# Optimization experiments

Measured on AMD Instinct MI355X. Metric: run time of the kernel, lower is better.

Reference implementation:

```python
import jax, jax.numpy as jnp
import numpy as np

B, N_MM, N_V, N_A = 2, 256, 64, 128
DIM, HEADS, ATTN_RATIO, MLP_RATIO = 1024, 16, 0.25, 4.0
INNER = int(DIM * ATTN_RATIO)          # 256
HID = int(DIM * MLP_RATIO)             # 4096
SCALE = (DIM // HEADS) ** -0.5         # faithful to source: uses dim//num_heads
EPS = 1e-5


def setup_inputs() -> dict:
    key = jax.random.key(0)
    ks = jax.random.split(key, 16)
    s = 0.02
    return {
        "xmm": jax.random.normal(ks[0], (B, N_MM, DIM), jnp.float32),
        "xv": jax.random.normal(ks[1], (B, N_V, DIM), jnp.float32),
        "xa": jax.random.normal(ks[2], (B, N_A, DIM), jnp.float32),
        "ln_mm_w": jnp.ones((DIM,), jnp.float32),
        "ln_mm_b": jnp.zeros((DIM,), jnp.float32),
        "ln_v_w": jnp.ones((DIM,), jnp.float32),
        "ln_v_b": jnp.zeros((DIM,), jnp.float32),
        "ln_a_w": jnp.ones((DIM,), jnp.float32),
        "ln_a_b": jnp.zeros((DIM,), jnp.float32),
        "Wq": jax.random.normal(ks[3], (DIM, INNER), jnp.float32) * s,
        "Wkv": jax.random.normal(ks[4], (2 * DIM, 2 * INNER), jnp.float32) * s,
        "Wproj": jax.random.normal(ks[5], (INNER, DIM), jnp.float32) * s,
        "bproj": jnp.zeros((DIM,), jnp.float32),
        "ln_mlp_w": jnp.ones((DIM,), jnp.float32),
        "ln_mlp_b": jnp.zeros((DIM,), jnp.float32),
        "W1": jax.random.normal(ks[6], (DIM, HID), jnp.float32) * s,
        "b1": jnp.zeros((HID,), jnp.float32),
        "W2": jax.random.normal(ks[7], (HID, DIM), jnp.float32) * s,
        "b2": jnp.zeros((DIM,), jnp.float32),
    }


def _ln(x, w, b):
    m = x.mean(-1, keepdims=True)
    v = ((x - m) ** 2).mean(-1, keepdims=True)
    return (x - m) / jnp.sqrt(v + EPS) * w + b


def reference(xmm, xv, xa, ln_mm_w, ln_mm_b, ln_v_w, ln_v_b, ln_a_w, ln_a_b,
              Wq, Wkv, Wproj, bproj, ln_mlp_w, ln_mlp_b, W1, b1, W2, b2):
    hd = INNER // HEADS
    src_mm = _ln(xmm, ln_mm_w, ln_mm_b)
    src_v = _ln(xv, ln_v_w, ln_v_b)
    src_a = _ln(xa, ln_a_w, ln_a_b)

    # kv(x_va) where x_va = cat([xv broadcast over N_a, xa broadcast over N_v], -1).
    # Equivalent to projecting each stream separately and broadcast-adding:
    kv_v = src_v @ Wkv[:DIM]            # [B, N_v, 2*INNER]
    kv_a = src_a @ Wkv[DIM:]            # [B, N_a, 2*INNER]
    kv = kv_v[:, :, None, :] + kv_a[:, None, :, :]          # [B, N_v, N_a, 2*INNER]
    kv = kv.reshape(B, N_V * N_A, 2, HEADS, hd)
    k = kv[:, :, 0].transpose(0, 2, 1, 3)                   # [B, H, N_va, hd]
    v = kv[:, :, 1].transpose(0, 2, 1, 3)

    q = (src_mm @ Wq).reshape(B, N_MM, HEADS, hd).transpose(0, 2, 1, 3)

    attn = jnp.einsum('bhqd,bhkd->bhqk', q, k) * SCALE
    attn = jax.nn.softmax(attn, axis=-1)
    out = jnp.einsum('bhqk,bhkd->bhqd', attn, v)
    out = out.transpose(0, 2, 1, 3).reshape(B, N_MM, INNER)
    out = out @ Wproj + bproj

    xmm = xmm + out
    h = _ln(xmm, ln_mlp_w, ln_mlp_b)
    h = jax.nn.gelu(h @ W1 + b1, approximate=False) @ W2 + b2
    return xmm + h
```

## Files before the change

kernel.cpp:

```cpp
#include <hip/hip_runtime.h>
#include <hip/hip_bf16.h>
#include <math.h>


typedef unsigned short ushort_t;
typedef __attribute__((ext_vector_type(8))) __bf16 bf16x8;
typedef __attribute__((ext_vector_type(4))) float f32x4;

#define DEVFN static __device__ __forceinline__

DEVFN ushort_t f2bf(float f) {
    unsigned int x = __float_as_uint(f);
    unsigned int r = x + 0x7FFFu + ((x >> 16) & 1u);
    return (ushort_t)(r >> 16);
}
DEVFN void unpack8(uint4 dv, float* dst) {
    unsigned int ws[4] = {dv.x, dv.y, dv.z, dv.w};
#pragma unroll
    for (int i = 0; i < 4; i++) {
        dst[2 * i] = __uint_as_float(ws[i] << 16);
        dst[2 * i + 1] = __uint_as_float(ws[i] & 0xFFFF0000u);
    }
}

DEVFN void ln_body(const float* __restrict__ x, const float* __restrict__ w,
                   const float* __restrict__ b, ushort_t* __restrict__ out,
                   int row) {
    const float4* xr4 = (const float4*)(x + (size_t)row * 1024);
    ushort_t* orow = out + (size_t)row * 1024;
    int tid = threadIdx.x;
    float4 v4 = xr4[tid];
    float s = v4.x + v4.y + v4.z + v4.w;
    float ss = v4.x * v4.x + v4.y * v4.y + v4.z * v4.z + v4.w * v4.w;
#pragma unroll
    for (int off = 32; off > 0; off >>= 1) {
        s += __shfl_down(s, off);
        ss += __shfl_down(ss, off);
    }
    __shared__ float red[8];
    if ((tid & 63) == 0) {
        red[tid >> 6] = s;
        red[4 + (tid >> 6)] = ss;
    }
    __syncthreads();
    s = red[0] + red[1] + red[2] + red[3];
    ss = red[4] + red[5] + red[6] + red[7];
    float mean = s * (1.f / 1024.f);
    float var = ss * (1.f / 1024.f) - mean * mean;
    float rstd = rsqrtf(var + 1e-5f);
    const float4 w4 = ((const float4*)w)[tid];
    const float4 b4 = ((const float4*)b)[tid];
    union { ushort_t u[4]; uint2 v; } pk;
    pk.u[0] = f2bf((v4.x - mean) * rstd * w4.x + b4.x);
    pk.u[1] = f2bf((v4.y - mean) * rstd * w4.y + b4.y);
    pk.u[2] = f2bf((v4.z - mean) * rstd * w4.z + b4.z);
    pk.u[3] = f2bf((v4.w - mean) * rstd * w4.w + b4.w);
    *(uint2*)(&orow[tid * 4]) = pk.v;
}

struct LNSeg {
    const float* x; const float* w; const float* b; ushort_t* out; int start;
};
struct TDesc { const float* in; ushort_t* out; int R, C, nx, start; };

DEVFN void transpose_body(TDesc d, int t, ushort_t* lds) {
    int bx = (t % d.nx) * 64;
    int by = (t / d.nx) * 64;
    int tid = threadIdx.x;
#pragma unroll
    for (int it = 0; it < 4; it++) {
        int idx = it * 256 + tid;
        int r = idx >> 4;
        int c4 = (idx & 15) << 2;
        float4 v = *(const float4*)(&d.in[(size_t)(by + r) * d.C + bx + c4]);
        float vals[4] = {v.x, v.y, v.z, v.w};
#pragma unroll
        for (int j = 0; j < 4; j++) {
            int c = c4 + j;
            int rs = (r + (((c >> 2) & 7) << 3)) & 63;
            lds[c * 64 + rs] = f2bf(vals[j]);
        }
    }
    __syncthreads();
#pragma unroll
    for (int it = 0; it < 2; it++) {
        int idx = it * 256 + tid;
        int c = idx >> 3;
        int l8 = idx & 7;
        int rs = ((l8 << 3) + (((c >> 2) & 7) << 3)) & 63;
        uint4 val = *(const uint4*)(&lds[c * 64 + rs]);
        *(uint4*)(&d.out[(size_t)(bx + c) * d.R + by + (l8 << 3)]) = val;
    }
    __syncthreads();
}

__global__ __launch_bounds__(256) void prep_kernel(LNSeg l0, LNSeg l1,
                                                   LNSeg l2, TDesc d0,
                                                   TDesc d1) {
    int id = blockIdx.x;
    if (id < 896) {
        LNSeg s = (id >= l2.start) ? l2 : ((id >= l1.start) ? l1 : l0);
        ln_body(s.x, s.w, s.b, s.out, id - s.start);
        return;
    }
    id -= 896;
    __shared__ ushort_t tile[64 * 64];
    TDesc d = (id >= d1.start) ? d1 : d0;
    transpose_body(d, id - d.start, tile);
}

template <int EPI, typename OutT>
DEVFN void gemm64_core(const ushort_t* __restrict__ A, int lda,
                       const ushort_t* __restrict__ B, int ldb,
                       OutT* __restrict__ C, int ldc,
                       const float* __restrict__ bias,
                       const float* __restrict__ resid, int K, int m0, int n0,
                       ushort_t* As, ushort_t* Bs,
                       float* __restrict__ stats = nullptr) {
    constexpr int LS = 72;
    int tid = threadIdx.x;
    int wave = tid >> 6, lane = tid & 63;
    int wm = wave >> 1, wn = wave & 1;
    int quad = lane >> 4, l16 = lane & 15;

    f32x4 acc[2][2];
#pragma unroll
    for (int i = 0; i < 2; i++)
#pragma unroll
        for (int j = 0; j < 2; j++) acc[i][j] = (f32x4){0.f, 0.f, 0.f, 0.f};

    int r = tid >> 3;
    int c = tid & 7;
    const ushort_t* Ap = A + (size_t)(m0 + r) * lda + c * 8;
    const ushort_t* Bp = B + (size_t)(n0 + r) * ldb + c * 8;
    const ushort_t* Ap2 = Ap + (size_t)32 * lda;
    const ushort_t* Bp2 = Bp + (size_t)32 * ldb;
    uint4 ra = *(const uint4*)Ap, ra2 = *(const uint4*)Ap2;
    uint4 rb = *(const uint4*)Bp, rb2 = *(const uint4*)Bp2;

    for (int k0 = 0; k0 < K; k0 += 64) {
        *(uint4*)(&As[r * LS + c * 8]) = ra;
        *(uint4*)(&As[(r + 32) * LS + c * 8]) = ra2;
        *(uint4*)(&Bs[r * LS + c * 8]) = rb;
        *(uint4*)(&Bs[(r + 32) * LS + c * 8]) = rb2;
        __syncthreads();
        if (k0 + 64 < K) {
            ra = *(const uint4*)(Ap + k0 + 64);
            ra2 = *(const uint4*)(Ap2 + k0 + 64);
            rb = *(const uint4*)(Bp + k0 + 64);
            rb2 = *(const uint4*)(Bp2 + k0 + 64);
        }
#pragma unroll
        for (int ks = 0; ks < 2; ks++) {
            bf16x8 af[2], bfr[2];
#pragma unroll
            for (int i = 0; i < 2; i++)
                af[i] = *(const bf16x8*)(
                    &As[(wm * 32 + i * 16 + l16) * LS + ks * 32 + quad * 8]);
#pragma unroll
            for (int j = 0; j < 2; j++)
                bfr[j] = *(const bf16x8*)(
                    &Bs[(wn * 32 + j * 16 + l16) * LS + ks * 32 + quad * 8]);
#pragma unroll
            for (int i = 0; i < 2; i++)
#pragma unroll
                for (int j = 0; j < 2; j++)
                    acc[i][j] = __builtin_amdgcn_mfma_f32_16x16x32_bf16(
                        af[i], bfr[j], acc[i][j], 0, 0, 0);
        }
        __syncthreads();
    }

    float srow[2][4] = {{0.f, 0.f, 0.f, 0.f}, {0.f, 0.f, 0.f, 0.f}};
    float ssrow[2][4] = {{0.f, 0.f, 0.f, 0.f}, {0.f, 0.f, 0.f, 0.f}};

#pragma unroll
    for (int i = 0; i < 2; i++)
#pragma unroll
        for (int j = 0; j < 2; j++) {
            int col = n0 + wn * 32 + j * 16 + l16;
            int rbase = m0 + wm * 32 + i * 16 + quad * 4;
            float bv = (EPI == 5) ? bias[col] : 0.f;
#pragma unroll
            for (int rr = 0; rr < 4; rr++) {
                int row = rbase + rr;
                float vv = acc[i][j][rr] + bv;
                if constexpr (EPI == 5) {
                    vv += resid[(size_t)row * ldc + col];
                    srow[i][rr] += vv;
                    ssrow[i][rr] += vv * vv;
                }
                if constexpr (sizeof(OutT) == 2)
                    C[(size_t)row * ldc + col] = (OutT)f2bf(vv);
                else
                    C[(size_t)row * ldc + col] = vv;
            }
        }

    if constexpr (EPI == 5) {
        float* ls = (float*)As;
#pragma unroll
        for (int i = 0; i < 2; i++)
#pragma unroll
            for (int rr = 0; rr < 4; rr++) {
                float s = srow[i][rr], ss = ssrow[i][rr];
#pragma unroll
                for (int m = 1; m < 16; m <<= 1) {
                    s += __shfl_xor(s, m);
                    ss += __shfl_xor(ss, m);
                }
                if (l16 == 0) {
                    int rl = wm * 32 + i * 16 + quad * 4 + rr;
                    ls[rl * 4 + wn * 2 + 0] = s;
                    ls[rl * 4 + wn * 2 + 1] = ss;
                }
            }
        __syncthreads();
        if (tid < 64) {
            float s = ls[tid * 4 + 0] + ls[tid * 4 + 2];
            float ss = ls[tid * 4 + 1] + ls[tid * 4 + 3];
            stats[(size_t)(m0 + tid) * 2 + 0] = s;
            stats[(size_t)(m0 + tid) * 2 + 1] = ss;
        }
    }
}

struct GSeg {
    const ushort_t* A; const ushort_t* B; ushort_t* C;
    int lda, ldb, ldc, nx, start;
};

__global__ __launch_bounds__(256) void projT_kernel(GSeg s0, GSeg s1, GSeg s2,
                                                    TDesc d0, TDesc d1,
                                                    TDesc d2, int K) {
    __shared__ ushort_t As[64 * 72];
    __shared__ ushort_t Bs[64 * 72];
    int id = blockIdx.x;
    if (id < 80) {
        GSeg s = (id >= s2.start) ? s2 : ((id >= s1.start) ? s1 : s0);
        int t = id - s.start;
        int n0 = (t % s.nx) * 64;
        int m0 = (t / s.nx) * 64;
        gemm64_core<0, ushort_t>(s.A, s.lda, s.B, s.ldb, s.C, s.ldc, nullptr,
                                 nullptr, K, m0, n0, As, Bs);
        return;
    }
    id -= 80;
    TDesc d = (id >= d2.start) ? d2 : ((id >= d1.start) ? d1 : d0);
    transpose_body(d, id - d.start, As);
}

__global__ __launch_bounds__(256) void ygemm_kernel(
    const ushort_t* __restrict__ A, const ushort_t* __restrict__ Bt,
    float* __restrict__ y, const float* __restrict__ bproj,
    const float* __restrict__ xmm, float* __restrict__ pstats) {
    __shared__ ushort_t As[64 * 72];
    __shared__ ushort_t Bs[64 * 72];
    gemm64_core<5, float>(A, 256, Bt, 256, y, 1024, bproj, xmm, 256,
                          blockIdx.y * 64, blockIdx.x * 64, As, Bs,
                          pstats + (size_t)blockIdx.x * 512 * 2);
}

__global__ __launch_bounds__(256) void mlp1_kernel(
    const float* __restrict__ y, const float* __restrict__ pstats,
    const float* __restrict__ lnw, const float* __restrict__ lnb,
    const ushort_t* __restrict__ W1t, const float* __restrict__ b1,
    ushort_t* __restrict__ g) {
    constexpr int LS = 40;
    __shared__ ushort_t As[64 * LS];
    __shared__ ushort_t Bs[64 * LS];
    __shared__ float wls[1024], bls[1024];
    int tid = threadIdx.x;
    int m0 = blockIdx.y * 64, n0 = blockIdx.x * 64;

    ((float4*)wls)[tid] = ((const float4*)lnw)[tid];
    ((float4*)bls)[tid] = ((const float4*)lnb)[tid];

    int r = tid >> 2, c = tid & 3;
    float s = 0.f, ss = 0.f;
#pragma unroll
    for (int k = 0; k < 4; k++) {
        size_t o = ((size_t)(c * 4 + k) * 512 + (m0 + r)) * 2;
        s += pstats[o];
        ss += pstats[o + 1];
    }
    s += __shfl_xor(s, 1); ss += __shfl_xor(ss, 1);
    s += __shfl_xor(s, 2); ss += __shfl_xor(ss, 2);
    float mr = s * (1.f / 1024.f);
    float var = ss * (1.f / 1024.f) - mr * mr;
    float rs = rsqrtf(var + 1e-5f);

    int wave = tid >> 6, lane = tid & 63;
    int wm = wave >> 1, wn = wave & 1;
    int quad = lane >> 4, l16 = lane & 15;

    f32x4 acc[2][2];
#pragma unroll
    for (int i = 0; i < 2; i++)
#pragma unroll
        for (int j = 0; j < 2; j++) acc[i][j] = (f32x4){0.f, 0.f, 0.f, 0.f};

    const float* Ay = y + (size_t)(m0 + r) * 1024 + c * 8;
    const ushort_t* Bp = W1t + (size_t)(n0 + r) * 1024 + c * 8;
    float4 ya0 = *(const float4*)Ay;
    float4 ya1 = *(const float4*)(Ay + 4);
    uint4 rb = *(const uint4*)Bp;
    __syncthreads();

    for (int k0 = 0; k0 < 1024; k0 += 32) {
        float4 w0 = *(const float4*)&wls[k0 + c * 8];
        float4 w1 = *(const float4*)&wls[k0 + c * 8 + 4];
        float4 bb0 = *(const float4*)&bls[k0 + c * 8];
        float4 bb1 = *(const float4*)&bls[k0 + c * 8 + 4];
        union { ushort_t u[8]; uint4 v; } pa;
        pa.u[0] = f2bf((ya0.x - mr) * rs * w0.x + bb0.x);
        pa.u[1] = f2bf((ya0.y - mr) * rs * w0.y + bb0.y);
        pa.u[2] = f2bf((ya0.z - mr) * rs * w0.z + bb0.z);
        pa.u[3] = f2bf((ya0.w - mr) * rs * w0.w + bb0.w);
        pa.u[4] = f2bf((ya1.x - mr) * rs * w1.x + bb1.x);
        pa.u[5] = f2bf((ya1.y - mr) * rs * w1.y + bb1.y);
        pa.u[6] = f2bf((ya1.z - mr) * rs * w1.z + bb1.z);
        pa.u[7] = f2bf((ya1.w - mr) * rs * w1.w + bb1.w);
        *(uint4*)(&As[r * LS + c * 8]) = pa.v;
        *(uint4*)(&Bs[r * LS + c * 8]) = rb;
        __syncthreads();
        if (k0 + 32 < 1024) {
            ya0 = *(const float4*)(Ay + k0 + 32);
            ya1 = *(const float4*)(Ay + k0 + 36);
            rb = *(const uint4*)(Bp + k0 + 32);
        }
        bf16x8 af[2], bfr[2];
#pragma unroll
        for (int i = 0; i < 2; i++)
            af[i] = *(const bf16x8*)(&As[(wm * 32 + i * 16 + l16) * LS + quad * 8]);
#pragma unroll
        for (int j = 0; j < 2; j++)
            bfr[j] = *(const bf16x8*)(&Bs[(wn * 32 + j * 16 + l16) * LS + quad * 8]);
#pragma unroll
        for (int i = 0; i < 2; i++)
#pragma unroll
            for (int j = 0; j < 2; j++)
                acc[i][j] = __builtin_amdgcn_mfma_f32_16x16x32_bf16(
                    af[i], bfr[j], acc[i][j], 0, 0, 0);
        __syncthreads();
    }

#pragma unroll
    for (int i = 0; i < 2; i++)
#pragma unroll
        for (int j = 0; j < 2; j++) {
            int col = n0 + wn * 32 + j * 16 + l16;
            int rbase = m0 + wm * 32 + i * 16 + quad * 4;
            float bv = b1[col];
#pragma unroll
            for (int rr = 0; rr < 4; rr++) {
                int row = rbase + rr;
                float vv = acc[i][j][rr] + bv;
                vv = 0.5f * vv * (1.f + erff(vv * 0.70710678118654752f));
                g[(size_t)row * 4096 + col] = f2bf(vv);
            }
        }
}

__global__ __launch_bounds__(256) void mlp2_kernel(
    const ushort_t* __restrict__ g, const ushort_t* __restrict__ W2t,
    float* __restrict__ P, const float* __restrict__ y,
    const float* __restrict__ b2, float* __restrict__ out,
    unsigned int* __restrict__ cnt) {
    __shared__ ushort_t As[64 * 72];
    __shared__ ushort_t Bs[64 * 72];
    int z = blockIdx.z;
    int m0 = blockIdx.y * 64, n0 = blockIdx.x * 64;
    gemm64_core<4, float>(g + (size_t)z * 1024, 4096, W2t + (size_t)z * 1024,
                          4096, P + (size_t)z * 512 * 1024, 1024, nullptr,
                          nullptr, 1024, m0, n0, As, Bs);

    __shared__ int lastf;
    __syncthreads();
    if (threadIdx.x == 0) {
        __threadfence();
        unsigned int old = __hip_atomic_fetch_add(
            &cnt[blockIdx.y * 16 + blockIdx.x], 1u, __ATOMIC_ACQ_REL,
            __HIP_MEMORY_SCOPE_AGENT);
        lastf = (old == 3u);
        if (lastf) __threadfence();
    }
    __syncthreads();
    if (!lastf) return;

    int tid = threadIdx.x;
#pragma unroll
    for (int k = 0; k < 4; k++) {
        int idx4 = tid * 4 + k;
        int row = m0 + (idx4 >> 4);
        int c0 = n0 + (idx4 & 15) * 4;
        size_t off = (size_t)row * 1024 + c0;
        float4 a = *(const float4*)(P + off);
        float4 b = *(const float4*)(P + 524288 + off);
        float4 cc = *(const float4*)(P + 1048576 + off);
        float4 d = *(const float4*)(P + 1572864 + off);
        float4 yy = *(const float4*)(y + off);
        float4 bb = *(const float4*)(b2 + c0);
        float4 o;
        o.x = a.x + b.x + cc.x + d.x + yy.x + bb.x;
        o.y = a.y + b.y + cc.y + d.y + yy.y + bb.y;
        o.z = a.z + b.z + cc.z + d.z + yy.z + bb.z;
        o.w = a.w + b.w + cc.w + d.w + yy.w + bb.w;
        *(float4*)(out + off) = o;
    }
}

__global__ __launch_bounds__(256) void attn_kernel(
    const ushort_t* __restrict__ q, const ushort_t* __restrict__ kvv,
    const ushort_t* __restrict__ kva, ushort_t* __restrict__ out,
    unsigned int* __restrict__ cnt) {
    if (blockIdx.x == 0 && blockIdx.y == 0 && threadIdx.x < 128)
        cnt[threadIdx.x] = 0u;

    int bh = blockIdx.x;
    int b = bh >> 4, h = bh & 15;
    int tid = threadIdx.x;

    __shared__ float Kv[64][16], Vv[64][16], Ka[128][16], Va[128][16];

    {
        int row = tid >> 2, seg = (tid >> 1) & 1, half = tid & 1;
        const ushort_t* src =
            kvv + (size_t)(b * 64 + row) * 512 + seg * 256 + h * 16 + half * 8;
        float* dst = (seg ? Vv[row] : Kv[row]) + half * 8;
        unpack8(*(const uint4*)src, dst);
    }
#pragma unroll
    for (int t2 = 0; t2 < 2; t2++) {
        int t = tid + t2 * 256;
        int row = t >> 2, seg = (t >> 1) & 1, half = t & 1;
        const ushort_t* src =
            kva + (size_t)(b * 128 + row) * 512 + seg * 256 + h * 16 + half * 8;
        float* dst = (seg ? Va[row] : Ka[row]) + half * 8;
        unpack8(*(const uint4*)src, dst);
    }
    __syncthreads();

    int qlocal = tid >> 2;
    int dg = tid & 3;
    int qrow = blockIdx.y * 64 + qlocal;
    const ushort_t* qp = q + (size_t)(b * 256 + qrow) * 256 + h * 16 + dg * 4;
    uint2 qu = *(const uint2*)qp;
    float4 qv;
    qv.x = __uint_as_float(qu.x << 16) * 0.125f;
    qv.y = __uint_as_float(qu.x & 0xFFFF0000u) * 0.125f;
    qv.z = __uint_as_float(qu.y << 16) * 0.125f;
    qv.w = __uint_as_float(qu.y & 0xFFFF0000u) * 0.125f;

    const float4* Kv4 = (const float4*)Kv;
    const float4* Vv4 = (const float4*)Vv;
    const float4* Ka4 = (const float4*)Ka;
    const float4* Va4 = (const float4*)Va;

    float4 ov = {0.f, 0.f, 0.f, 0.f};
    float den = 0.f;
#pragma unroll 8
    for (int i = 0; i < 64; i++) {
        float4 kk = Kv4[i * 4 + dg];
        float part = qv.x * kk.x + qv.y * kk.y + qv.z * kk.z + qv.w * kk.w;
        part += __shfl_xor(part, 1);
        part += __shfl_xor(part, 2);
        float p = __expf(part);
        den += p;
        float4 vv = Vv4[i * 4 + dg];
        ov.x += p * vv.x; ov.y += p * vv.y; ov.z += p * vv.z; ov.w += p * vv.w;
    }
    float4 oa = {0.f, 0.f, 0.f, 0.f};
    float dena = 0.f;
#pragma unroll 8
    for (int i = 0; i < 128; i++) {
        float4 kk = Ka4[i * 4 + dg];
        float part = qv.x * kk.x + qv.y * kk.y + qv.z * kk.z + qv.w * kk.w;
        part += __shfl_xor(part, 1);
        part += __shfl_xor(part, 2);
        float p = __expf(part);
        dena += p;
        float4 vv = Va4[i * 4 + dg];
        oa.x += p * vv.x; oa.y += p * vv.y; oa.z += p * vv.z; oa.w += p * vv.w;
    }

    float rv = 1.f / den, ra = 1.f / dena;
    union { ushort_t u[4]; uint2 v; } pk;
    pk.u[0] = f2bf(ov.x * rv + oa.x * ra);
    pk.u[1] = f2bf(ov.y * rv + oa.y * ra);
    pk.u[2] = f2bf(ov.z * rv + oa.z * ra);
    pk.u[3] = f2bf(ov.w * rv + oa.w * ra);
    *(uint2*)(out + (size_t)(b * 256 + qrow) * 256 + h * 16 + dg * 4) = pk.v;
}

extern "C" void kernel_launch(void* const* d_in, const int* in_sizes, int n_in,
                              void* d_out, int out_size, void* d_ws,
                              size_t ws_size, hipStream_t stream) {
    const float* xmm = (const float*)d_in[0];
    const float* xv = (const float*)d_in[1];
    const float* xa = (const float*)d_in[2];
    const float* ln_mm_w = (const float*)d_in[3];
    const float* ln_mm_b = (const float*)d_in[4];
    const float* ln_v_w = (const float*)d_in[5];
    const float* ln_v_b = (const float*)d_in[6];
    const float* ln_a_w = (const float*)d_in[7];
    const float* ln_a_b = (const float*)d_in[8];
    const float* Wq = (const float*)d_in[9];
    const float* Wkv = (const float*)d_in[10];
    const float* Wproj = (const float*)d_in[11];
    const float* bproj = (const float*)d_in[12];
    const float* ln_mlp_w = (const float*)d_in[13];
    const float* ln_mlp_b = (const float*)d_in[14];
    const float* W1 = (const float*)d_in[15];
    const float* b1 = (const float*)d_in[16];
    const float* W2 = (const float*)d_in[17];
    const float* b2 = (const float*)d_in[18];
    float* outp = (float*)d_out;

    char* w = (char*)d_ws;
    unsigned int* cnt = (unsigned int*)w; w += 1024;
    float* pstats = (float*)w;        w += 16 * 512 * 2 * 4;
    ushort_t* xmmN = (ushort_t*)w;    w += 512 * 1024 * 2;
    ushort_t* xvN = (ushort_t*)w;     w += 128 * 1024 * 2;
    ushort_t* xaN = (ushort_t*)w;     w += 256 * 1024 * 2;
    ushort_t* Wqt = (ushort_t*)w;     w += 256 * 1024 * 2;
    ushort_t* Wkvt = (ushort_t*)w;    w += 512 * 2048 * 2;
    ushort_t* Wprojt = (ushort_t*)w;  w += 1024 * 256 * 2;
    ushort_t* W1t = (ushort_t*)w;     w += 4096 * 1024 * 2;
    ushort_t* W2t = (ushort_t*)w;     w += 1024 * 4096 * 2;
    ushort_t* qout = (ushort_t*)w;    w += 512 * 256 * 2;
    ushort_t* kvvb = (ushort_t*)w;    w += 128 * 512 * 2;
    ushort_t* kvab = (ushort_t*)w;    w += 256 * 512 * 2;
    ushort_t* attnout = (ushort_t*)w; w += 512 * 256 * 2;
    float* y = (float*)w;             w += 512 * 1024 * 4;
    ushort_t* g = (ushort_t*)w;       w += 512 * 4096 * 2;
    float* P = (float*)w;             w += 4 * 512 * 1024 * 4;

    LNSeg L0{xmm, ln_mm_w, ln_mm_b, xmmN, 0};
    LNSeg L1{xv, ln_v_w, ln_v_b, xvN, 512};
    LNSeg L2{xa, ln_a_w, ln_a_b, xaN, 640};
    TDesc TQ{Wq, Wqt, 1024, 256, 4, 0};
    TDesc TKV{Wkv, Wkvt, 2048, 512, 8, 64};
    prep_kernel<<<896 + 320, 256, 0, stream>>>(L0, L1, L2, TQ, TKV);

    GSeg G0{xmmN, Wqt, qout, 1024, 1024, 256, 4, 0};
    GSeg G1{xvN, Wkvt, kvvb, 1024, 2048, 512, 8, 32};
    GSeg G2{xaN, Wkvt + 1024, kvab, 1024, 2048, 512, 8, 48};
    TDesc TP{Wproj, Wprojt, 256, 1024, 16, 0};
    TDesc T1{W1, W1t, 1024, 4096, 64, 64};
    TDesc T2{W2, W2t, 4096, 1024, 16, 1088};
    projT_kernel<<<80 + 2112, 256, 0, stream>>>(G0, G1, G2, TP, T1, T2, 1024);

    attn_kernel<<<dim3(32, 4), 256, 0, stream>>>(qout, kvvb, kvab, attnout,
                                                 cnt);

    ygemm_kernel<<<dim3(16, 8), 256, 0, stream>>>(attnout, Wprojt, y, bproj,
                                                  xmm, pstats);

    mlp1_kernel<<<dim3(64, 8), 256, 0, stream>>>(y, pstats, ln_mlp_w,
                                                 ln_mlp_b, W1t, b1, g);

    mlp2_kernel<<<dim3(16, 8, 4), 256, 0, stream>>>(g, W2t, P, y, b2, outp,
                                                    cnt);

    (void)in_sizes; (void)n_in; (void)out_size; (void)ws_size;
}
```

Measured before the change: 224.0 us.

## Widen mlp1 K-tile to 64 and split mlp2 split-K reduction into separate kernel

The fused-LayerNorm MLP1 GEMM now stages a 64-wide K slice per iteration, two rows per thread, with two MFMA k-steps per stage. This halves the number of barrier pairs and loop trips at the cost of more shared memory and registers. MLP2 drops its atomic-counter last-block reduction in favour of a plain split-K GEMM followed by a separate elementwise reduce kernel. That removes the atomics and the counter reset in the attention kernel but adds one launch and a full extra pass over the partial sums.

```diff
diff --git a/kernel.cpp b/kernel.cpp
--- a/kernel.cpp
+++ b/kernel.cpp
@@ -225,6 +225,19 @@
     }
 }
 
+template <int EPI, typename OutT>
+__global__ __launch_bounds__(256) void gemm64(
+    const ushort_t* __restrict__ A, int lda, const ushort_t* __restrict__ Bt,
+    int ldb, OutT* __restrict__ C, int ldc, const float* __restrict__ bias,
+    const float* __restrict__ resid, int Kper, int sliceStride) {
+    __shared__ ushort_t As[64 * 72];
+    __shared__ ushort_t Bs[64 * 72];
+    int z = blockIdx.z;
+    gemm64_core<EPI, OutT>(A + (size_t)z * Kper, lda, Bt + (size_t)z * Kper,
+                           ldb, C + (size_t)z * sliceStride, ldc, bias, resid,
+                           Kper, blockIdx.y * 64, blockIdx.x * 64, As, Bs);
+}
+
 struct GSeg {
     const ushort_t* A; const ushort_t* B; ushort_t* C;
     int lda, ldb, ldc, nx, start;
@@ -266,29 +279,35 @@
     const float* __restrict__ lnw, const float* __restrict__ lnb,
     const ushort_t* __restrict__ W1t, const float* __restrict__ b1,
     ushort_t* __restrict__ g) {
-    constexpr int LS = 40;
+    constexpr int LS = 72;
     __shared__ ushort_t As[64 * LS];
     __shared__ ushort_t Bs[64 * LS];
     __shared__ float wls[1024], bls[1024];
+    __shared__ float meanv[64], rstdv[64];
     int tid = threadIdx.x;
     int m0 = blockIdx.y * 64, n0 = blockIdx.x * 64;
 
     ((float4*)wls)[tid] = ((const float4*)lnw)[tid];
     ((float4*)bls)[tid] = ((const float4*)lnb)[tid];
 
-    int r = tid >> 2, c = tid & 3;
-    float s = 0.f, ss = 0.f;
-#pragma unroll
-    for (int k = 0; k < 4; k++) {
-        size_t o = ((size_t)(c * 4 + k) * 512 + (m0 + r)) * 2;
-        s += pstats[o];
-        ss += pstats[o + 1];
-    }
-    s += __shfl_xor(s, 1); ss += __shfl_xor(ss, 1);
-    s += __shfl_xor(s, 2); ss += __shfl_xor(ss, 2);
-    float mr = s * (1.f / 1024.f);
-    float var = ss * (1.f / 1024.f) - mr * mr;
-    float rs = rsqrtf(var + 1e-5f);
+    {
+        int row = tid >> 2, q = tid & 3;
+        float s = 0.f, ss = 0.f;
+#pragma unroll
+        for (int k = 0; k < 4; k++) {
+            size_t o = ((size_t)(q * 4 + k) * 512 + (m0 + row)) * 2;
+            s += pstats[o];
+            ss += pstats[o + 1];
+        }
+        s += __shfl_xor(s, 1); ss += __shfl_xor(ss, 1);
+        s += __shfl_xor(s, 2); ss += __shfl_xor(ss, 2);
+        if (q == 0) {
+            float mean = s * (1.f / 1024.f);
+            float var = ss * (1.f / 1024.f) - mean * mean;
+            meanv[row] = mean;
+            rstdv[row] = rsqrtf(var + 1e-5f);
+        }
+    }
 
     int wave = tid >> 6, lane = tid & 63;
     int wm = wave >> 1, wn = wave & 1;
@@ -300,48 +319,77 @@
 #pragma unroll
         for (int j = 0; j < 2; j++) acc[i][j] = (f32x4){0.f, 0.f, 0.f, 0.f};
 
+    int r = tid >> 3;
+    int c = tid & 7;
     const float* Ay = y + (size_t)(m0 + r) * 1024 + c * 8;
+    const float* Ay2 = Ay + (size_t)32 * 1024;
     const ushort_t* Bp = W1t + (size_t)(n0 + r) * 1024 + c * 8;
-    float4 ya0 = *(const float4*)Ay;
-    float4 ya1 = *(const float4*)(Ay + 4);
+    const ushort_t* Bp2 = Bp + (size_t)32 * 1024;
+
+    __syncthreads();
+    float mr0 = meanv[r], rs0 = rstdv[r];
+    float mr1 = meanv[r + 32], rs1 = rstdv[r + 32];
+
+    float4 a00 = *(const float4*)(Ay);
+    float4 a01 = *(const float4*)(Ay + 4);
+    float4 a10 = *(const float4*)(Ay2);
+    float4 a11 = *(const float4*)(Ay2 + 4);
     uint4 rb = *(const uint4*)Bp;
-    __syncthreads();
-
-    for (int k0 = 0; k0 < 1024; k0 += 32) {
+    uint4 rb2 = *(const uint4*)Bp2;
+
+    for (int k0 = 0; k0 < 1024; k0 += 64) {
         float4 w0 = *(const float4*)&wls[k0 + c * 8];
         float4 w1 = *(const float4*)&wls[k0 + c * 8 + 4];
         float4 bb0 = *(const float4*)&bls[k0 + c * 8];
         float4 bb1 = *(const float4*)&bls[k0 + c * 8 + 4];
-        union { ushort_t u[8]; uint4 v; } pa;
-        pa.u[0] = f2bf((ya0.x - mr) * rs * w0.x + bb0.x);
-        pa.u[1] = f2bf((ya0.y - mr) * rs * w0.y + bb0.y);
-        pa.u[2] = f2bf((ya0.z - mr) * rs * w0.z + bb0.z);
-        pa.u[3] = f2bf((ya0.w - mr) * rs * w0.w + bb0.w);
-        pa.u[4] = f2bf((ya1.x - mr) * rs * w1.x + bb1.x);
-        pa.u[5] = f2bf((ya1.y - mr) * rs * w1.y + bb1.y);
-        pa.u[6] = f2bf((ya1.z - mr) * rs * w1.z + bb1.z);
-        pa.u[7] = f2bf((ya1.w - mr) * rs * w1.w + bb1.w);
-        *(uint4*)(&As[r * LS + c * 8]) = pa.v;
+        union { ushort_t u[8]; uint4 v; } p0, p1;
+        p0.u[0] = f2bf((a00.x - mr0) * rs0 * w0.x + bb0.x);
+        p0.u[1] = f2bf((a00.y - mr0) * rs0 * w0.y + bb0.y);
+        p0.u[2] = f2bf((a00.z - mr0) * rs0 * w0.z + bb0.z);
+        p0.u[3] = f2bf((a00.w - mr0) * rs0 * w0.w + bb0.w);
+        p0.u[4] = f2bf((a01.x - mr0) * rs0 * w1.x + bb1.x);
+        p0.u[5] = f2bf((a01.y - mr0) * rs0 * w1.y + bb1.y);
+        p0.u[6] = f2bf((a01.z - mr0) * rs0 * w1.z + bb1.z);
+        p0.u[7] = f2bf((a01.w - mr0) * rs0 * w1.w + bb1.w);
+        p1.u[0] = f2bf((a10.x - mr1) * rs1 * w0.x + bb0.x);
+        p1.u[1] = f2bf((a10.y - mr1) * rs1 * w0.y + bb0.y);
+        p1.u[2] = f2bf((a10.z - mr1) * rs1 * w0.z + bb0.z);
+        p1.u[3] = f2bf((a10.w - mr1) * rs1 * w0.w + bb0.w);
+        p1.u[4] = f2bf((a11.x - mr1) * rs1 * w1.x + bb1.x);
+        p1.u[5] = f2bf((a11.y - mr1) * rs1 * w1.y + bb1.y);
+        p1.u[6] = f2bf((a11.z - mr1) * rs1 * w1.z + bb1.z);
+        p1.u[7] = f2bf((a11.w - mr1) * rs1 * w1.w + bb1.w);
+        *(uint4*)(&As[r * LS + c * 8]) = p0.v;
+        *(uint4*)(&As[(r + 32) * LS + c * 8]) = p1.v;
         *(uint4*)(&Bs[r * LS + c * 8]) = rb;
+        *(uint4*)(&Bs[(r + 32) * LS + c * 8]) = rb2;
         __syncthreads();
-        if (k0 + 32 < 1024) {
-            ya0 = *(const float4*)(Ay + k0 + 32);
-            ya1 = *(const float4*)(Ay + k0 + 36);
-            rb = *(const uint4*)(Bp + k0 + 32);
-        }
-        bf16x8 af[2], bfr[2];
-#pragma unroll
-        for (int i = 0; i < 2; i++)
-            af[i] = *(const bf16x8*)(&As[(wm * 32 + i * 16 + l16) * LS + quad * 8]);
-#pragma unroll
-        for (int j = 0; j < 2; j++)
-            bfr[j] = *(const bf16x8*)(&Bs[(wn * 32 + j * 16 + l16) * LS + quad * 8]);
-#pragma unroll
-        for (int i = 0; i < 2; i++)
+        if (k0 + 64 < 1024) {
+            a00 = *(const float4*)(Ay + k0 + 64);
+            a01 = *(const float4*)(Ay + k0 + 68);
+            a10 = *(const float4*)(Ay2 + k0 + 64);
+            a11 = *(const float4*)(Ay2 + k0 + 68);
+            rb = *(const uint4*)(Bp + k0 + 64);
+            rb2 = *(const uint4*)(Bp2 + k0 + 64);
+        }
+#pragma unroll
+        for (int ks = 0; ks < 2; ks++) {
+            bf16x8 af[2], bfr[2];
+#pragma unroll
+            for (int i = 0; i < 2; i++)
+                af[i] = *(const bf16x8*)(
+                    &As[(wm * 32 + i * 16 + l16) * LS + ks * 32 + quad * 8]);
 #pragma unroll
             for (int j = 0; j < 2; j++)
-                acc[i][j] = __builtin_amdgcn_mfma_f32_16x16x32_bf16(
-                    af[i], bfr[j], acc[i][j], 0, 0, 0);
+                bfr[j] = *(const bf16x8*)(
+                    &Bs[(wn * 32 + j * 16 + l16) * LS + ks * 32 + quad * 8]);
+#pragma unroll
+            for (int i = 0; i < 2; i++)
+#pragma unroll
+                for (int j = 0; j < 2; j++)
+                    acc[i][j] = __builtin_amdgcn_mfma_f32_16x16x32_bf16(
+                        af[i], bfr[j], acc[i][j], 0, 0, 0);
+        }
         __syncthreads();
     }
 
@@ -362,61 +410,26 @@
         }
 }
 
-__global__ __launch_bounds__(256) void mlp2_kernel(
-    const ushort_t* __restrict__ g, const ushort_t* __restrict__ W2t,
-    float* __restrict__ P, const float* __restrict__ y,
-    const float* __restrict__ b2, float* __restrict__ out,
-    unsigned int* __restrict__ cnt) {
-    __shared__ ushort_t As[64 * 72];
-    __shared__ ushort_t Bs[64 * 72];
-    int z = blockIdx.z;
-    int m0 = blockIdx.y * 64, n0 = blockIdx.x * 64;
-    gemm64_core<4, float>(g + (size_t)z * 1024, 4096, W2t + (size_t)z * 1024,
-                          4096, P + (size_t)z * 512 * 1024, 1024, nullptr,
-                          nullptr, 1024, m0, n0, As, Bs);
-
-    __shared__ int lastf;
-    __syncthreads();
-    if (threadIdx.x == 0) {
-        __threadfence();
-        unsigned int old = __hip_atomic_fetch_add(
-            &cnt[blockIdx.y * 16 + blockIdx.x], 1u, __ATOMIC_ACQ_REL,
-            __HIP_MEMORY_SCOPE_AGENT);
-        lastf = (old == 3u);
-        if (lastf) __threadfence();
-    }
-    __syncthreads();
-    if (!lastf) return;
-
-    int tid = threadIdx.x;
-#pragma unroll
-    for (int k = 0; k < 4; k++) {
-        int idx4 = tid * 4 + k;
-        int row = m0 + (idx4 >> 4);
-        int c0 = n0 + (idx4 & 15) * 4;
-        size_t off = (size_t)row * 1024 + c0;
-        float4 a = *(const float4*)(P + off);
-        float4 b = *(const float4*)(P + 524288 + off);
-        float4 cc = *(const float4*)(P + 1048576 + off);
-        float4 d = *(const float4*)(P + 1572864 + off);
-        float4 yy = *(const float4*)(y + off);
-        float4 bb = *(const float4*)(b2 + c0);
-        float4 o;
-        o.x = a.x + b.x + cc.x + d.x + yy.x + bb.x;
-        o.y = a.y + b.y + cc.y + d.y + yy.y + bb.y;
-        o.z = a.z + b.z + cc.z + d.z + yy.z + bb.z;
-        o.w = a.w + b.w + cc.w + d.w + yy.w + bb.w;
-        *(float4*)(out + off) = o;
-    }
+__global__ __launch_bounds__(256) void reduce_mlp2(
+    const float* __restrict__ P, const float* __restrict__ y,
+    const float* __restrict__ b2, float* __restrict__ out) {
+    int i = blockIdx.x * 256 + threadIdx.x;
+    const float4* p = (const float4*)P;
+    float4 a = p[i], b = p[i + 131072], cc = p[i + 2 * 131072],
+           d = p[i + 3 * 131072];
+    float4 yy = ((const float4*)y)[i];
+    float4 bb = ((const float4*)b2)[i & 255];
+    float4 o;
+    o.x = a.x + b.x + cc.x + d.x + yy.x + bb.x;
+    o.y = a.y + b.y + cc.y + d.y + yy.y + bb.y;
+    o.z = a.z + b.z + cc.z + d.z + yy.z + bb.z;
+    o.w = a.w + b.w + cc.w + d.w + yy.w + bb.w;
+    ((float4*)out)[i] = o;
 }
 
 __global__ __launch_bounds__(256) void attn_kernel(
     const ushort_t* __restrict__ q, const ushort_t* __restrict__ kvv,
-    const ushort_t* __restrict__ kva, ushort_t* __restrict__ out,
-    unsigned int* __restrict__ cnt) {
-    if (blockIdx.x == 0 && blockIdx.y == 0 && threadIdx.x < 128)
-        cnt[threadIdx.x] = 0u;
-
+    const ushort_t* __restrict__ kva, ushort_t* __restrict__ out) {
     int bh = blockIdx.x;
     int b = bh >> 4, h = bh & 15;
     int tid = threadIdx.x;
@@ -518,7 +531,6 @@
     float* outp = (float*)d_out;
 
     char* w = (char*)d_ws;
-    unsigned int* cnt = (unsigned int*)w; w += 1024;
     float* pstats = (float*)w;        w += 16 * 512 * 2 * 4;
     ushort_t* xmmN = (ushort_t*)w;    w += 512 * 1024 * 2;
     ushort_t* xvN = (ushort_t*)w;     w += 128 * 1024 * 2;
@@ -551,8 +563,7 @@
     TDesc T2{W2, W2t, 4096, 1024, 16, 1088};
     projT_kernel<<<80 + 2112, 256, 0, stream>>>(G0, G1, G2, TP, T1, T2, 1024);
 
-    attn_kernel<<<dim3(32, 4), 256, 0, stream>>>(qout, kvvb, kvab, attnout,
-                                                 cnt);
+    attn_kernel<<<dim3(32, 4), 256, 0, stream>>>(qout, kvvb, kvab, attnout);
 
     ygemm_kernel<<<dim3(16, 8), 256, 0, stream>>>(attnout, Wprojt, y, bproj,
                                                   xmm, pstats);
@@ -560,8 +571,10 @@
     mlp1_kernel<<<dim3(64, 8), 256, 0, stream>>>(y, pstats, ln_mlp_w,
                                                  ln_mlp_b, W1t, b1, g);
 
-    mlp2_kernel<<<dim3(16, 8, 4), 256, 0, stream>>>(g, W2t, P, y, b2, outp,
-                                                    cnt);
+    gemm64<4, float><<<dim3(16, 8, 4), 256, 0, stream>>>(
+        g, 4096, W2t, 4096, P, 1024, nullptr, nullptr, 1024, 512 * 1024);
+
+    reduce_mlp2<<<512, 256, 0, stream>>>(P, y, b2, outp);
 
     (void)in_sizes; (void)n_in; (void)out_size; (void)ws_size;
 }
```

After: 189.1 us. 15.6% less time.
